# Kernel tuning notes

Measured on AMD Instinct MI355X. Metric: run time of the kernel, lower is better.

## Reference

```python
import jax, jax.numpy as jnp
import numpy as np

DIM = 1024
N_HEADS = 16
HEAD_DIM = DIM // N_HEADS
HIDDEN = 4 * DIM
B, T = 4, 2048
EPS = 1e-5


def setup_inputs() -> dict:
    key = jax.random.key(0)
    ks = jax.random.split(key, 12)
    s = lambda fan_in: 1.0 / np.sqrt(fan_in)
    return {
        "x": jax.random.normal(ks[0], (B, T, DIM), jnp.float32),
        "ln1_g": jnp.ones((DIM,), jnp.float32),
        "ln1_b": jnp.zeros((DIM,), jnp.float32),
        "qkv_w": jax.random.normal(ks[1], (DIM, 3 * DIM), jnp.float32) * s(DIM),
        "qkv_b": jnp.zeros((3 * DIM,), jnp.float32),
        "proj_w": jax.random.normal(ks[2], (DIM, DIM), jnp.float32) * s(DIM),
        "proj_b": jnp.zeros((DIM,), jnp.float32),
        "ln2_g": jnp.ones((DIM,), jnp.float32),
        "ln2_b": jnp.zeros((DIM,), jnp.float32),
        "ff1_w": jax.random.normal(ks[3], (DIM, HIDDEN), jnp.float32) * s(DIM),
        "ff1_b": jnp.zeros((HIDDEN,), jnp.float32),
        "ff2_w": jax.random.normal(ks[4], (HIDDEN, DIM), jnp.float32) * s(HIDDEN),
        "ff2_b": jnp.zeros((DIM,), jnp.float32),
    }


def _layernorm(x, g, b):
    mu = jnp.mean(x, axis=-1, keepdims=True)
    var = jnp.mean(jnp.square(x - mu), axis=-1, keepdims=True)
    return (x - mu) * jax.lax.rsqrt(var + EPS) * g + b


def _attn(x, qkv_w, qkv_b, proj_w, proj_b):
    Bx, Tx, C = x.shape
    qkv = (x @ qkv_w + qkv_b).reshape(Bx, Tx, 3, N_HEADS, HEAD_DIM)
    q, k, v = (qkv[:, :, i].transpose(0, 2, 1, 3) for i in range(3))  # [B,H,T,hd]
    att = jnp.einsum('bhqd,bhkd->bhqk', q, k) / np.sqrt(HEAD_DIM)
    causal = jnp.tril(jnp.ones((Tx, Tx), bool))
    att = jnp.where(causal, att, -jnp.inf)
    att = jax.nn.softmax(att, axis=-1)
    out = jnp.einsum('bhqk,bhkd->bhqd', att, v).transpose(0, 2, 1, 3).reshape(Bx, Tx, C)
    return out @ proj_w + proj_b


def reference(x, ln1_g, ln1_b, qkv_w, qkv_b, proj_w, proj_b,
              ln2_g, ln2_b, ff1_w, ff1_b, ff2_w, ff2_b):
    x = x + _attn(_layernorm(x, ln1_g, ln1_b), qkv_w, qkv_b, proj_w, proj_b)
    h = _layernorm(x, ln2_g, ln2_b)
    h = jax.nn.gelu(h @ ff1_w + ff1_b, approximate=False) @ ff2_w + ff2_b
    return x + h
```

## Files before the change

### kernel.cpp

```cpp
#include <hip/hip_runtime.h>
#include <hip/hip_bf16.h>
#include <math.h>

#define DIM 1024
#define NHEADS 16
#define HD 64
#define TT 2048
#define BB 4
#define MTOK (BB*TT)
#define HID 4096

typedef __attribute__((ext_vector_type(8))) short bf16x8;
typedef __attribute__((ext_vector_type(4))) float f32x4;
typedef unsigned short u16;
typedef unsigned int u32;

__device__ inline u16 f2b(float f){
  __hip_bfloat16 h = __float2bfloat16(f);
  return __builtin_bit_cast(u16, h);
}

__device__ inline u32 cvtpk(float lo, float hi_){
  u32 r;
  asm("v_cvt_pk_bf16_f32 %0, %1, %2" : "=v"(r) : "v"(lo), "v"(hi_));
  return r;
}

__device__ inline void load_lds16(const void* g, void* l){
  __builtin_amdgcn_global_load_lds(
      (const __attribute__((address_space(1))) void*)g,
      (__attribute__((address_space(3))) void*)l,
      16, 0, 0);
}

__global__ __launch_bounds__(256) void wconv_t(const float* __restrict__ W,
                                               u16* __restrict__ Wt, int K, int N){
  __shared__ float tl[32][33];
  const int k0 = blockIdx.x*32, n0 = blockIdx.y*32;
  const int tx = threadIdx.x & 31, ty = threadIdx.x >> 5;
  #pragma unroll
  for (int r=0;r<32;r+=8)
    tl[ty+r][tx] = W[(size_t)(k0+ty+r)*N + (n0+tx)];
  __syncthreads();
  #pragma unroll
  for (int r=0;r<32;r+=8)
    Wt[(size_t)(n0+ty+r)*K + (k0+tx)] = f2b(tl[tx][ty+r]);
}

__global__ __launch_bounds__(256) void ln_fwd(const float* __restrict__ x,
                                              const float* __restrict__ g,
                                              const float* __restrict__ bta,
                                              u16* __restrict__ out){
  const int row = blockIdx.x, t = threadIdx.x;
  const float4 v = ((const float4*)(x + (size_t)row*DIM))[t];
  float s  = v.x+v.y+v.z+v.w;
  float s2 = v.x*v.x+v.y*v.y+v.z*v.z+v.w*v.w;
  #pragma unroll
  for (int m=1;m<64;m<<=1){ s += __shfl_xor(s,m); s2 += __shfl_xor(s2,m); }
  __shared__ float red[8];
  if ((t&63)==0){ red[t>>6]=s; red[4+(t>>6)]=s2; }
  __syncthreads();
  s  = red[0]+red[1]+red[2]+red[3];
  s2 = red[4]+red[5]+red[6]+red[7];
  const float mu = s*(1.0f/DIM);
  const float rstd = rsqrtf(s2*(1.0f/DIM) - mu*mu + 1e-5f);
  const float4 gv = ((const float4*)g)[t];
  const float4 bv = ((const float4*)bta)[t];
  ushort4 ov;
  ov.x = f2b((v.x-mu)*rstd*gv.x + bv.x);
  ov.y = f2b((v.y-mu)*rstd*gv.y + bv.y);
  ov.z = f2b((v.z-mu)*rstd*gv.z + bv.z);
  ov.w = f2b((v.w-mu)*rstd*gv.w + bv.w);
  ((ushort4*)out)[(size_t)row*(DIM/4) + t] = ov;
}

template<int EPI>
__global__ __launch_bounds__(256) void gemm_bt(
    const u16* __restrict__ A, const u16* __restrict__ Bt,
    const float* __restrict__ bias, const float* __restrict__ resid,
    float* __restrict__ outf, u16* __restrict__ outh,
    u16* __restrict__ qo, u16* __restrict__ ko, u16* __restrict__ vo,
    int M, int N, int K)
{
  __shared__ __align__(16) u16 smem[16384];
  u16* As = smem;
  u16* Bs = smem + 8192;
  u16* Ct = smem;
  const int t = threadIdx.x, wv = t>>6, ln = t&63;
  const int nbx = gridDim.x, nwg = nbx*gridDim.y;
  const int bid = blockIdx.y*nbx + blockIdx.x;
  const int cpx = nwg>>3;
  const int wid = (bid&7)*cpx + (bid>>3);
  const int m0 = (wid/nbx)*128, n0 = (wid%nbx)*128;
  const int wr = wv>>1, wc = wv&1;
  const int hi = ln>>4, lr = hi*4, lc = ln&15;
  f32x4 acc[4][4] = {};

  int rdoff[2];
  #pragma unroll
  for (int kk=0; kk<2; kk++)
    rdoff[kk] = ((kk*4 + hi) ^ (lc&7)) << 3;

  for (int kt=0; kt<K; kt+=64){
    #pragma unroll
    for (int j=0;j<4;j++){
      const int chunk = j*256 + t;
      const int row = chunk>>3;
      const int cS  = (chunk&7) ^ (row&7);
      load_lds16(A  + (size_t)(m0+row)*K + kt + cS*8, (char*)As + chunk*16);
      load_lds16(Bt + (size_t)(n0+row)*K + kt + cS*8, (char*)Bs + chunk*16);
    }
    asm volatile("s_waitcnt vmcnt(0)" ::: "memory");
    __syncthreads();
    bf16x8 af[4][2], bfr[4][2];
    #pragma unroll
    for (int mi=0;mi<4;mi++){
      const int rbase = (wr*64 + mi*16 + lc) << 6;
      af[mi][0] = *(const bf16x8*)&As[rbase + rdoff[0]];
      af[mi][1] = *(const bf16x8*)&As[rbase + rdoff[1]];
    }
    #pragma unroll
    for (int ni=0;ni<4;ni++){
      const int rbase = (wc*64 + ni*16 + lc) << 6;
      bfr[ni][0] = *(const bf16x8*)&Bs[rbase + rdoff[0]];
      bfr[ni][1] = *(const bf16x8*)&Bs[rbase + rdoff[1]];
    }
    #pragma unroll
    for (int kk=0;kk<2;kk++)
      #pragma unroll
      for (int mi=0;mi<4;mi++)
        #pragma unroll
        for (int ni=0;ni<4;ni++)
          acc[mi][ni] = __builtin_amdgcn_mfma_f32_16x16x32_bf16(af[mi][kk], bfr[ni][kk], acc[mi][ni], 0,0,0);
    __syncthreads();
  }

  if constexpr (EPI==1 || EPI==3){
    #pragma unroll
    for (int ni=0;ni<4;ni++){
      const int gn = n0 + wc*64 + ni*16 + lc;
      const float bv = bias[gn];
      #pragma unroll
      for (int mi=0;mi<4;mi++){
        const int gmb = m0 + wr*64 + mi*16 + lr;
        f32x4 a = acc[mi][ni];
        #pragma unroll
        for (int i=0;i<4;i++){
          const size_t idx = (size_t)(gmb+i)*DIM + gn;
          outf[idx] = a[i] + bv + resid[idx];
        }
      }
    }
  } else {
    const int part = (EPI==0) ? (n0>>10) : 0;
    __syncthreads();
    #pragma unroll
    for (int ni=0;ni<4;ni++){
      const int gn = n0 + wc*64 + ni*16 + lc;
      const float bv = bias[gn];
      const int cl = wc*64 + ni*16 + lc;
      #pragma unroll
      for (int mi=0;mi<4;mi++){
        f32x4 a = acc[mi][ni];
        #pragma unroll
        for (int i=0;i<4;i++){
          const int rl = wr*64 + mi*16 + lr + i;
          float val = a[i] + bv;
          if constexpr (EPI==2){
            const float xx = val*val;
            const float w  = val * fmaf(xx, 0.10294322f, 2.30220781f);
            const float y  = exp2f(w);
            const float r_ = __builtin_amdgcn_rcpf(1.0f + y);
            val = val - val*r_;
          }
          int r = rl, c = cl;
          if (EPI==0 && part==2){ r = cl; c = rl; }
          const int chunk = c>>3;
          const int csw = (chunk&8) | ((chunk ^ (r&7)) & 7);
          Ct[(r<<7) + (csw<<3) + (c&7)] = f2b(val);
        }
      }
    }
    __syncthreads();
    const int cid = t & 7, rsub = t >> 3;
    const int bb = m0>>11, tok0b = m0&2047;
    const int h0 = (EPI==0) ? ((n0&1023)>>6) : 0;
    #pragma unroll
    for (int pass=0; pass<4; ++pass){
      const int rr = pass*32 + rsub;
      #pragma unroll
      for (int hh=0; hh<2; ++hh){
        const int chunk = hh*8 + cid;
        const int sw = (chunk&8) | ((chunk ^ (rr&7)) & 7);
        const bf16x8 vvv = *(const bf16x8*)&Ct[(rr<<7) + (sw<<3)];
        if constexpr (EPI==2){
          *(bf16x8*)&outh[(size_t)(m0+rr)*HID + n0 + chunk*8] = vvv;
        } else {
          if (part==2){
            const int head = h0 + (rr>>6), d = rr&63;
            *(bf16x8*)&vo[(((size_t)bb*NHEADS + head)*HD + d)*TT + tok0b + chunk*8] = vvv;
          } else {
            u16* dst = part ? ko : qo;
            const int head = h0 + hh;
            *(bf16x8*)&dst[(((size_t)bb*NHEADS + head)*TT + tok0b + rr)*HD + cid*8] = vvv;
          }
        }
      }
    }
  }
}

__global__ __launch_bounds__(512) void attn_fwd(
    const u16* __restrict__ qpt, const u16* __restrict__ kb, const u16* __restrict__ vtb,
    u16* __restrict__ o)
{
  __shared__ __align__(16) u16 Kd[2][64*64];
  __shared__ __align__(16) u16 Vd[2][64*64];
  const int t = threadIdx.x, wv = t>>6, ln = t&63;
  const int bid  = blockIdx.y*gridDim.x + blockIdx.x;
  const int orig = (bid&7)*64 + (bid>>3);
  const int bh   = orig>>3;
  const int qp   = orig&7;
  const int qbA  = qp, qbB = 15-qp;
  const size_t base = (size_t)bh*TT*HD;
  const int hi = ln>>4, lc = ln&15;
  const int ntA = 2*qbA + 2, ntB = 2*qbB + 2;
  const int qbaseA = qbA*128 + wv*16, qrowA = qbaseA + lc;
  const int qbaseB = qbB*128 + wv*16, qrowB = qbaseB + lc;

  const bf16x8 qfA0 = *(const bf16x8*)(qpt + base + (size_t)qrowA*HD + hi*8);
  const bf16x8 qfA1 = *(const bf16x8*)(qpt + base + (size_t)qrowA*HD + 32 + hi*8);
  const bf16x8 qfB0 = *(const bf16x8*)(qpt + base + (size_t)qrowB*HD + hi*8);
  const bf16x8 qfB1 = *(const bf16x8*)(qpt + base + (size_t)qrowB*HD + 32 + hi*8);
  f32x4 oaccA[4] = {}, oaccB[4] = {};
  f32x4 lsumA = {0.f,0.f,0.f,0.f}, lsumB = {0.f,0.f,0.f,0.f};
  float mrunA = -1e30f, mrunB = -1e30f;
  const float SCQ = 0.125f * 1.44269504f;
  bf16x8 ones;
  #pragma unroll
  for (int j=0;j<8;j++) ones[j] = (short)0x3F80;

  const int srow = t>>3;
  const int sch  = t&7;
  const int gch  = (sch ^ (srow&7))<<3;

  auto STAGE = [&](int nb, int kt){
    load_lds16(kb  + base + (size_t)(kt*64+srow)*HD + gch, &Kd[nb][srow*64 + sch*8]);
    load_lds16(vtb + base + (size_t)srow*TT + kt*64 + gch, &Vd[nb][srow*64 + sch*8]);
  };
  auto FRAG = [&](const u16* buf, int r, int ch)->bf16x8{
    return *(const bf16x8*)(buf + r*64 + ((ch ^ (r&7))<<3));
  };
  const int src0 = ((ln&16)<<1) + lc;
  const int src1 = src0 + 16;
  auto pick = [&](u32 w0, u32 w1, int src)->u32{
    const u32 a = (u32)__shfl((int)w0, src);
    const u32 b = (u32)__shfl((int)w1, src);
    return (hi<2) ? a : b;
  };

  auto strip_tile = [&](int kt, const u16* Kb, const u16* Vb,
                        const bf16x8& qf0, const bf16x8& qf1,
                        int qbase, int qrow,
                        f32x4* oacc, f32x4& lsum, float& mrun){
    if (kt*64 > qbase + 15) return;
    float sv[4][4];
    __builtin_amdgcn_s_setprio(1);
    #pragma unroll
    for (int cf=0;cf<4;cf++){
      const int r = cf*16 + lc;
      const bf16x8 kf0 = FRAG(Kb, r, hi);
      const bf16x8 kf1 = FRAG(Kb, r, hi+4);
      f32x4 z = {0.f,0.f,0.f,0.f};
      z = __builtin_amdgcn_mfma_f32_16x16x32_bf16(kf0, qf0, z, 0,0,0);
      z = __builtin_amdgcn_mfma_f32_16x16x32_bf16(kf1, qf1, z, 0,0,0);
      sv[cf][0]=z[0]; sv[cf][1]=z[1]; sv[cf][2]=z[2]; sv[cf][3]=z[3];
    }
    __builtin_amdgcn_s_setprio(0);
    float mx = -1e30f;
    if (kt*64 + 63 > qbase){
      #pragma unroll
      for (int cf=0;cf<4;cf++)
        #pragma unroll
        for (int i=0;i<4;i++){
          const int kvg = kt*64 + cf*16 + 4*hi + i;
          float s_ = sv[cf][i]*SCQ;
          s_ = (kvg > qrow) ? -1e30f : s_;
          sv[cf][i] = s_;
          mx = fmaxf(mx, s_);
        }
    } else {
      #pragma unroll
      for (int cf=0;cf<4;cf++)
        #pragma unroll
        for (int i=0;i<4;i++){
          const float s_ = sv[cf][i]*SCQ;
          sv[cf][i] = s_;
          mx = fmaxf(mx, s_);
        }
    }
    mx = fmaxf(mx, __shfl_xor(mx, 16));
    mx = fmaxf(mx, __shfl_xor(mx, 32));
    if (__any(mx > mrun + 11.0f)){
      const float mnew = fmaxf(mrun, mx);
      const float sc = exp2f(mrun - mnew);
      mrun = mnew;
      const float s0 = __shfl(sc, 4*hi+0);
      const float s1 = __shfl(sc, 4*hi+1);
      const float s2 = __shfl(sc, 4*hi+2);
      const float s3 = __shfl(sc, 4*hi+3);
      #pragma unroll
      for (int df=0;df<4;df++){
        oacc[df][0] *= s0; oacc[df][1] *= s1;
        oacc[df][2] *= s2; oacc[df][3] *= s3;
      }
      lsum[0] *= s0; lsum[1] *= s1; lsum[2] *= s2; lsum[3] *= s3;
    }
    u32 W[4][2];
    #pragma unroll
    for (int cf=0;cf<4;cf++){
      const float e0 = exp2f(sv[cf][0] - mrun);
      const float e1 = exp2f(sv[cf][1] - mrun);
      const float e2 = exp2f(sv[cf][2] - mrun);
      const float e3 = exp2f(sv[cf][3] - mrun);
      W[cf][0] = cvtpk(e0, e1);
      W[cf][1] = cvtpk(e2, e3);
    }
    uint4 uA, uB;
    uA.x = pick(W[0][0], W[1][0], src0);
    uA.y = pick(W[0][1], W[1][1], src0);
    uA.z = pick(W[0][0], W[1][0], src1);
    uA.w = pick(W[0][1], W[1][1], src1);
    uB.x = pick(W[2][0], W[3][0], src0);
    uB.y = pick(W[2][1], W[3][1], src0);
    uB.z = pick(W[2][0], W[3][0], src1);
    uB.w = pick(W[2][1], W[3][1], src1);
    const bf16x8 paA = __builtin_bit_cast(bf16x8, uA);
    const bf16x8 paB = __builtin_bit_cast(bf16x8, uB);
    __builtin_amdgcn_s_setprio(1);
    #pragma unroll
    for (int df=0;df<4;df++){
      const bf16x8 v0 = FRAG(Vb, df*16+lc, hi);
      const bf16x8 v1 = FRAG(Vb, df*16+lc, hi+4);
      oacc[df] = __builtin_amdgcn_mfma_f32_16x16x32_bf16(paA, v0, oacc[df], 0,0,0);
      oacc[df] = __builtin_amdgcn_mfma_f32_16x16x32_bf16(paB, v1, oacc[df], 0,0,0);
    }
    lsum = __builtin_amdgcn_mfma_f32_16x16x32_bf16(paA, ones, lsum, 0,0,0);
    lsum = __builtin_amdgcn_mfma_f32_16x16x32_bf16(paB, ones, lsum, 0,0,0);
    __builtin_amdgcn_s_setprio(0);
  };

  int cur = 0;
  STAGE(0, 0);
  asm volatile("s_waitcnt vmcnt(0)" ::: "memory");
  __syncthreads();

  for (int kt=0; kt<ntB; kt++){
    if (kt+1 < ntB) STAGE(cur^1, kt+1);
    const u16* Kb = Kd[cur];
    const u16* Vb = Vd[cur];
    strip_tile(kt, Kb, Vb, qfB0, qfB1, qbaseB, qrowB, oaccB, lsumB, mrunB);
    if (kt < ntA)
      strip_tile(kt, Kb, Vb, qfA0, qfA1, qbaseA, qrowA, oaccA, lsumA, mrunA);
    asm volatile("s_waitcnt vmcnt(0)" ::: "memory");
    __syncthreads();
    cur ^= 1;
  }

  const int b = bh>>4, h = bh&15;
  {
    const float inv[4] = {1.0f/lsumA[0], 1.0f/lsumA[1], 1.0f/lsumA[2], 1.0f/lsumA[3]};
    const int qg0 = qbaseA + 4*hi;
    #pragma unroll
    for (int i=0;i<4;i++){
      const size_t rowb = ((size_t)b*TT + (size_t)(qg0 + i))*DIM + h*HD;
      #pragma unroll
      for (int df=0;df<4;df++)
        o[rowb + df*16 + lc] = f2b(oaccA[df][i]*inv[i]);
    }
  }
  {
    const float inv[4] = {1.0f/lsumB[0], 1.0f/lsumB[1], 1.0f/lsumB[2], 1.0f/lsumB[3]};
    const int qg0 = qbaseB + 4*hi;
    #pragma unroll
    for (int i=0;i<4;i++){
      const size_t rowb = ((size_t)b*TT + (size_t)(qg0 + i))*DIM + h*HD;
      #pragma unroll
      for (int df=0;df<4;df++)
        o[rowb + df*16 + lc] = f2b(oaccB[df][i]*inv[i]);
    }
  }
}

extern "C" void kernel_launch(void* const* d_in, const int* in_sizes, int n_in,
                              void* d_out, int out_size, void* d_ws, size_t ws_size,
                              hipStream_t stream){
  (void)in_sizes; (void)n_in; (void)out_size; (void)ws_size;
  const float* x     = (const float*)d_in[0];
  const float* ln1g  = (const float*)d_in[1];
  const float* ln1b  = (const float*)d_in[2];
  const float* qkvw  = (const float*)d_in[3];
  const float* qkvb  = (const float*)d_in[4];
  const float* projw = (const float*)d_in[5];
  const float* projb = (const float*)d_in[6];
  const float* ln2g  = (const float*)d_in[7];
  const float* ln2b  = (const float*)d_in[8];
  const float* ff1w  = (const float*)d_in[9];
  const float* ff1b  = (const float*)d_in[10];
  const float* ff2w  = (const float*)d_in[11];
  const float* ff2b  = (const float*)d_in[12];
  float* out = (float*)d_out;

  char* ws = (char*)d_ws;
  size_t off = 0;
  auto alloc = [&](size_t n){ char* p = ws + off; off += (n + 255) & ~(size_t)255; return p; };
  u16* wqkvt  = (u16*)alloc((size_t)3072*1024*2);
  u16* wprojt = (u16*)alloc((size_t)1024*1024*2);
  u16* wff1t  = (u16*)alloc((size_t)4096*1024*2);
  u16* wff2t  = (u16*)alloc((size_t)1024*4096*2);
  u16* h1     = (u16*)alloc((size_t)MTOK*DIM*2);
  u16* qbuf   = (u16*)alloc((size_t)MTOK*DIM*2);
  u16* kbuf   = (u16*)alloc((size_t)MTOK*DIM*2);
  u16* vbuf   = (u16*)alloc((size_t)MTOK*DIM*2);
  u16* aout   = (u16*)alloc((size_t)MTOK*DIM*2);
  float* x2   = (float*)alloc((size_t)MTOK*DIM*4);
  u16* h2     = (u16*)alloc((size_t)MTOK*DIM*2);
  u16* act    = (u16*)alloc((size_t)MTOK*HID*2);

  wconv_t<<<dim3(1024/32, 3072/32), 256, 0, stream>>>(qkvw, wqkvt, 1024, 3072);
  wconv_t<<<dim3(1024/32, 1024/32), 256, 0, stream>>>(projw, wprojt, 1024, 1024);
  wconv_t<<<dim3(1024/32, 4096/32), 256, 0, stream>>>(ff1w, wff1t, 1024, 4096);
  wconv_t<<<dim3(4096/32, 1024/32), 256, 0, stream>>>(ff2w, wff2t, 4096, 1024);

  ln_fwd<<<MTOK, 256, 0, stream>>>(x, ln1g, ln1b, h1);

  gemm_bt<0><<<dim3(3072/128, MTOK/128), 256, 0, stream>>>(
      h1, wqkvt, qkvb, nullptr, nullptr, nullptr, qbuf, kbuf, vbuf, MTOK, 3072, 1024);

  attn_fwd<<<dim3(8, BB*NHEADS), 512, 0, stream>>>(qbuf, kbuf, vbuf, aout);

  gemm_bt<1><<<dim3(1024/128, MTOK/128), 256, 0, stream>>>(
      aout, wprojt, projb, x, x2, nullptr, nullptr, nullptr, nullptr, MTOK, 1024, 1024);

  ln_fwd<<<MTOK, 256, 0, stream>>>(x2, ln2g, ln2b, h2);

  gemm_bt<2><<<dim3(4096/128, MTOK/128), 256, 0, stream>>>(
      h2, wff1t, ff1b, nullptr, nullptr, act, nullptr, nullptr, nullptr, MTOK, HID, 1024);

  gemm_bt<3><<<dim3(1024/128, MTOK/128), 256, 0, stream>>>(
      act, wff2t, ff2b, x2, out, nullptr, nullptr, nullptr, nullptr, MTOK, DIM, HID);
}
```

Before: 436.9 us.

## Double-buffer LDS tiles in proj and FF2 GEMMs to overlap loads with MFMA

Adds a DBUF template path to the GEMM that stages the next K-tile into a second LDS buffer while MFMAs run on the current one, leaving one barrier per iteration instead of two. It is enabled only for the N=1024 GEMMs (projection and FF2), which launch fewer workgroups and have a long K in FF2. The QKV and FF1 GEMMs keep single buffering. LDS use doubles to 64KB per block, which may lower occupancy and limit latency hiding across workgroups.

```diff
diff --git a/kernel.cpp b/kernel.cpp
--- a/kernel.cpp
+++ b/kernel.cpp
@@ -74,7 +74,7 @@
   ((ushort4*)out)[(size_t)row*(DIM/4) + t] = ov;
 }
 
-template<int EPI>
+template<int EPI, bool DBUF>
 __global__ __launch_bounds__(256) void gemm_bt(
     const u16* __restrict__ A, const u16* __restrict__ Bt,
     const float* __restrict__ bias, const float* __restrict__ resid,
@@ -82,9 +82,7 @@
     u16* __restrict__ qo, u16* __restrict__ ko, u16* __restrict__ vo,
     int M, int N, int K)
 {
-  __shared__ __align__(16) u16 smem[16384];
-  u16* As = smem;
-  u16* Bs = smem + 8192;
+  __shared__ __align__(16) u16 smem[DBUF ? 32768 : 16384];
   u16* Ct = smem;
   const int t = threadIdx.x, wv = t>>6, ln = t&63;
   const int nbx = gridDim.x, nwg = nbx*gridDim.y;
@@ -101,7 +99,9 @@
   for (int kk=0; kk<2; kk++)
     rdoff[kk] = ((kk*4 + hi) ^ (lc&7)) << 3;
 
-  for (int kt=0; kt<K; kt+=64){
+  auto STAGE = [&](int buf, int kt){
+    u16* As = smem + buf*16384;
+    u16* Bs = smem + buf*16384 + 8192;
     #pragma unroll
     for (int j=0;j<4;j++){
       const int chunk = j*256 + t;
@@ -110,8 +110,10 @@
       load_lds16(A  + (size_t)(m0+row)*K + kt + cS*8, (char*)As + chunk*16);
       load_lds16(Bt + (size_t)(n0+row)*K + kt + cS*8, (char*)Bs + chunk*16);
     }
-    asm volatile("s_waitcnt vmcnt(0)" ::: "memory");
-    __syncthreads();
+  };
+  auto COMPUTE = [&](int buf){
+    const u16* As = smem + buf*16384;
+    const u16* Bs = smem + buf*16384 + 8192;
     bf16x8 af[4][2], bfr[4][2];
     #pragma unroll
     for (int mi=0;mi<4;mi++){
@@ -132,7 +134,29 @@
         #pragma unroll
         for (int ni=0;ni<4;ni++)
           acc[mi][ni] = __builtin_amdgcn_mfma_f32_16x16x32_bf16(af[mi][kk], bfr[ni][kk], acc[mi][ni], 0,0,0);
+  };
+
+  if constexpr (DBUF){
+    STAGE(0, 0);
+    asm volatile("s_waitcnt vmcnt(0)" ::: "memory");
     __syncthreads();
+    int cur = 0;
+    for (int kt=64; kt<K; kt+=64){
+      STAGE(cur^1, kt);
+      COMPUTE(cur);
+      asm volatile("s_waitcnt vmcnt(0)" ::: "memory");
+      __syncthreads();
+      cur ^= 1;
+    }
+    COMPUTE(cur);
+  } else {
+    for (int kt=0; kt<K; kt+=64){
+      STAGE(0, kt);
+      asm volatile("s_waitcnt vmcnt(0)" ::: "memory");
+      __syncthreads();
+      COMPUTE(0);
+      __syncthreads();
+    }
   }
 
   if constexpr (EPI==1 || EPI==3){
@@ -434,19 +458,19 @@
 
   ln_fwd<<<MTOK, 256, 0, stream>>>(x, ln1g, ln1b, h1);
 
-  gemm_bt<0><<<dim3(3072/128, MTOK/128), 256, 0, stream>>>(
+  gemm_bt<0,false><<<dim3(3072/128, MTOK/128), 256, 0, stream>>>(
       h1, wqkvt, qkvb, nullptr, nullptr, nullptr, qbuf, kbuf, vbuf, MTOK, 3072, 1024);
 
   attn_fwd<<<dim3(8, BB*NHEADS), 512, 0, stream>>>(qbuf, kbuf, vbuf, aout);
 
-  gemm_bt<1><<<dim3(1024/128, MTOK/128), 256, 0, stream>>>(
+  gemm_bt<1,true><<<dim3(1024/128, MTOK/128), 256, 0, stream>>>(
       aout, wprojt, projb, x, x2, nullptr, nullptr, nullptr, nullptr, MTOK, 1024, 1024);
 
   ln_fwd<<<MTOK, 256, 0, stream>>>(x2, ln2g, ln2b, h2);
 
-  gemm_bt<2><<<dim3(4096/128, MTOK/128), 256, 0, stream>>>(
+  gemm_bt<2,false><<<dim3(4096/128, MTOK/128), 256, 0, stream>>>(
       h2, wff1t, ff1b, nullptr, nullptr, act, nullptr, nullptr, nullptr, MTOK, HID, 1024);
 
-  gemm_bt<3><<<dim3(1024/128, MTOK/128), 256, 0, stream>>>(
+  gemm_bt<3,true><<<dim3(1024/128, MTOK/128), 256, 0, stream>>>(
       act, wff2t, ff2b, x2, out, nullptr, nullptr, nullptr, nullptr, MTOK, DIM, HID);
 }
```

New measurement: 422.9 us. 1.03x faster.
